# Kernel optimization log

Measured on AMD Instinct MI355X. Metric: run time of the kernel, lower is better.

Reference implementation:

```python
import jax, jax.numpy as jnp
import numpy as np

DH = 5.0       # spatial grid spacing
DT = 0.002     # time step
C  = 2200.0    # wave speed


def setup_inputs() -> dict:
    key = jax.random.key(0)
    # (N, C=1, T, H, W) wavefield snapshots
    inputs = jax.random.normal(key, (8, 1, 64, 256, 256), dtype=jnp.float32)
    return {"inputs": inputs}


def reference(inputs):
    # Effective conv weight is (1,1,3,3,3): single-channel 3x3x3 stencils.
    # padding=(0,1,1): valid along depth (time), zero-pad 1 along H and W.
    u = inputs[:, 0]  # (N, T, H, W)
    up = jnp.pad(u, ((0, 0), (0, 0), (1, 1), (1, 1)))  # zero-pad H, W
    c0 = up[:, 1:-1, 1:-1, 1:-1]  # center tap, (N, T-2, H, W)
    inv_dh2 = 1.0 / (DH * DH)
    inv_dt2 = 1.0 / (DT * DT)
    # [1,-2,1] along W (conv_x kernel)
    u_dxdx = (up[:, 1:-1, 1:-1, :-2] - 2.0 * c0 + up[:, 1:-1, 1:-1, 2:]) * inv_dh2
    # [1,-2,1] along H (conv_y kernel)
    u_dydy = (up[:, 1:-1, :-2, 1:-1] - 2.0 * c0 + up[:, 1:-1, 2:, 1:-1]) * inv_dh2
    # [1,-2,1] along T (conv_z kernel, valid)
    u_dtdt = (up[:, :-2, 1:-1, 1:-1] - 2.0 * c0 + up[:, 2:, 1:-1, 1:-1]) * inv_dt2
    residuals = u_dxdx + u_dydy - u_dtdt * (1.0 / (C * C))
    # torch.norm -> Frobenius norm over all elements
    return jnp.sqrt(jnp.sum(residuals * residuals))
```

## Files before the change

kernel.cpp:

```cpp
#include <hip/hip_runtime.h>
#include <math.h>

#define B_    8
#define T_    64
#define NY_   256
#define NX_   256
#define PS_   (NY_ * NX_)

#define YB_     8
#define NSTRIP  (NY_ / YB_)
#define TCHUNKS 8
#define NWAVES  (B_ * NSTRIP * TCHUNKS)
#define NTHREADS 256
#define NBLOCKS  (NWAVES / 4)

__device__ __forceinline__ float4 loadf4(const float* p) { return *(const float4*)p; }

template <int LEN>
__device__ __forceinline__ float strip_accum(const float* __restrict__ u,
                                             int b, int ys, int t0, int lane) {
    const float a   = 0.04f;
    const float kdt = 250000.0f / 4840000.0f;
    const float k2  = 2.0f * kdt - 4.0f * a;

    const int y0 = ys * YB_;
    const float m0 = (ys > 0)           ? 1.0f : 0.0f;
    const float m5 = (ys < NSTRIP - 1)  ? 1.0f : 0.0f;
    const float xl = (lane > 0)  ? 1.0f : 0.0f;
    const float xr = (lane < 63) ? 1.0f : 0.0f;

    int yoff[YB_ + 2];
    #pragma unroll
    for (int j = 0; j < YB_ + 2; ++j) {
        int y = y0 - 1 + j;
        y = y < 0 ? 0 : (y > NY_ - 1 ? NY_ - 1 : y);
        yoff[j] = y * NX_;
    }

    const float* pl = u + ((size_t)b * T_ + t0) * PS_ + lane * 4;

    float4 tm[YB_], c[YB_ + 2];
    #pragma unroll
    for (int i = 0; i < YB_; ++i) tm[i] = loadf4(pl + yoff[i + 1]);
    const float* p1 = pl + PS_;
    #pragma unroll
    for (int j = 0; j < YB_ + 2; ++j) c[j] = loadf4(p1 + yoff[j]);
    c[0].x *= m0; c[0].y *= m0; c[0].z *= m0; c[0].w *= m0;
    c[YB_+1].x *= m5; c[YB_+1].y *= m5; c[YB_+1].z *= m5; c[YB_+1].w *= m5;

    float acc = 0.0f;
    const float* pn = pl + 2 * PS_;
    #pragma unroll
    for (int k = 0; k < LEN; ++k) {
        float4 nn[YB_ + 2];
        #pragma unroll
        for (int j = 0; j < YB_ + 2; ++j) nn[j] = loadf4(pn + yoff[j]);
        nn[0].x *= m0; nn[0].y *= m0; nn[0].z *= m0; nn[0].w *= m0;
        nn[YB_+1].x *= m5; nn[YB_+1].y *= m5; nn[YB_+1].z *= m5; nn[YB_+1].w *= m5;

        #pragma unroll
        for (int i = 0; i < YB_; ++i) {
            float4 ctr = c[i + 1], up = c[i], dn = c[i + 2];
            float4 t = tm[i], nf = nn[i + 1];
            float cl = __shfl_up(ctr.w, 1, 64) * xl;
            float cr = __shfl_down(ctr.x, 1, 64) * xr;

            {
                float s2 = cl + ctr.y + up.x + dn.x;
                float r = fmaf(s2, a, fmaf(t.x + nf.x, -kdt, ctr.x * k2));
                acc = fmaf(r, r, acc);
            }
            {
                float s2 = ctr.x + ctr.z + up.y + dn.y;
                float r = fmaf(s2, a, fmaf(t.y + nf.y, -kdt, ctr.y * k2));
                acc = fmaf(r, r, acc);
            }
            {
                float s2 = ctr.y + ctr.w + up.z + dn.z;
                float r = fmaf(s2, a, fmaf(t.z + nf.z, -kdt, ctr.z * k2));
                acc = fmaf(r, r, acc);
            }
            {
                float s2 = ctr.z + cr + up.w + dn.w;
                float r = fmaf(s2, a, fmaf(t.w + nf.w, -kdt, ctr.w * k2));
                acc = fmaf(r, r, acc);
            }
        }

        #pragma unroll
        for (int i = 0; i < YB_; ++i) tm[i] = c[i + 1];
        #pragma unroll
        for (int j = 0; j < YB_ + 2; ++j) c[j] = nn[j];
        pn += PS_;
    }
    return acc;
}

__global__ __launch_bounds__(NTHREADS, 2)
void pinn_residual_partial(const float* __restrict__ u, float* __restrict__ partial) {
    const int lane = threadIdx.x & 63;
    const int w    = threadIdx.x >> 6;

    const int b     = blockIdx.x & 7;
    const int inner = blockIdx.x >> 3;
    const int ys    = (inner & 7) * 4 + w;
    const int tc    = inner >> 3;
    const int t0    = tc * 8;

    float s;
    if (tc < TCHUNKS - 1) s = strip_accum<8>(u, b, ys, t0, lane);
    else                  s = strip_accum<6>(u, b, ys, t0, lane);

    #pragma unroll
    for (int off = 32; off > 0; off >>= 1)
        s += __shfl_down(s, off, 64);

    __shared__ float lds[NTHREADS / 64];
    if (lane == 0) lds[w] = s;
    __syncthreads();
    if (threadIdx.x == 0) {
        float bs = lds[0] + lds[1] + lds[2] + lds[3];
        partial[blockIdx.x] = bs;
    }
}

__global__ __launch_bounds__(NTHREADS)
void pinn_finalize(const float* __restrict__ partial, float* __restrict__ out) {
    float s = 0.0f;
    for (int i = threadIdx.x; i < NBLOCKS; i += NTHREADS)
        s += partial[i];
    #pragma unroll
    for (int off = 32; off > 0; off >>= 1)
        s += __shfl_down(s, off, 64);
    __shared__ float lds[NTHREADS / 64];
    int lane = threadIdx.x & 63;
    int wid  = threadIdx.x >> 6;
    if (lane == 0) lds[wid] = s;
    __syncthreads();
    if (threadIdx.x == 0) {
        float bs = 0.0f;
        #pragma unroll
        for (int q = 0; q < NTHREADS / 64; ++q) bs += lds[q];
        out[0] = sqrtf(bs);
    }
}

extern "C" void kernel_launch(void* const* d_in, const int* in_sizes, int n_in,
                              void* d_out, int out_size, void* d_ws, size_t ws_size,
                              hipStream_t stream) {
    const float* u = (const float*)d_in[0];
    float* partial = (float*)d_ws;
    float* out     = (float*)d_out;

    pinn_residual_partial<<<NBLOCKS, NTHREADS, 0, stream>>>(u, partial);
    pinn_finalize<<<1, NTHREADS, 0, stream>>>(partial, out);
}
```

Before: 31.18 us.

## Split each row strip into two x-halves with float2 loads and halo columns

Each wave now covers half a row (128 columns) with float2 loads instead of a full row with float4, so twice as many waves and blocks run. Each lane-0/lane-63 edge gets its neighbour from an extra scalar halo load per row, and the launch bound is raised to 4 blocks per CU so the lighter register footprint allows more occupancy. This is meant to expose more parallelism and latency hiding for a memory-bound stencil, at the cost of extra scalar halo loads and narrower vector accesses.

Result: slower. 43.19 us (+38.5%).

```diff
diff --git a/kernel.cpp b/kernel.cpp
--- a/kernel.cpp
+++ b/kernel.cpp
@@ -10,15 +10,16 @@
 #define YB_     8
 #define NSTRIP  (NY_ / YB_)
 #define TCHUNKS 8
-#define NWAVES  (B_ * NSTRIP * TCHUNKS)
+#define XH_     2
+#define NWAVES  (B_ * NSTRIP * TCHUNKS * XH_)
 #define NTHREADS 256
 #define NBLOCKS  (NWAVES / 4)
 
-__device__ __forceinline__ float4 loadf4(const float* p) { return *(const float4*)p; }
+__device__ __forceinline__ float2 loadf2(const float* p) { return *(const float2*)p; }
 
 template <int LEN>
 __device__ __forceinline__ float strip_accum(const float* __restrict__ u,
-                                             int b, int ys, int t0, int lane) {
+                                             int b, int ys, int t0, int xh, int lane) {
     const float a   = 0.04f;
     const float kdt = 250000.0f / 4840000.0f;
     const float k2  = 2.0f * kdt - 4.0f * a;
@@ -26,8 +27,9 @@
     const int y0 = ys * YB_;
     const float m0 = (ys > 0)           ? 1.0f : 0.0f;
     const float m5 = (ys < NSTRIP - 1)  ? 1.0f : 0.0f;
-    const float xl = (lane > 0)  ? 1.0f : 0.0f;
-    const float xr = (lane < 63) ? 1.0f : 0.0f;
+    const float ehl = (xh != 0) ? 1.0f : 0.0f;
+    const float ehr = 1.0f - ehl;
+    const int   ex  = xh ? 127 : 128;
 
     int yoff[YB_ + 2];
     #pragma unroll
@@ -37,33 +39,44 @@
         yoff[j] = y * NX_;
     }
 
-    const float* pl = u + ((size_t)b * T_ + t0) * PS_ + lane * 4;
+    const float* base = u + ((size_t)b * T_ + t0) * PS_;
+    const float* pl   = base + xh * 128 + lane * 2;
 
-    float4 tm[YB_], c[YB_ + 2];
+    float2 tm[YB_], c[YB_ + 2];
+    float  cE[YB_];
     #pragma unroll
-    for (int i = 0; i < YB_; ++i) tm[i] = loadf4(pl + yoff[i + 1]);
+    for (int i = 0; i < YB_; ++i) tm[i] = loadf2(pl + yoff[i + 1]);
     const float* p1 = pl + PS_;
     #pragma unroll
-    for (int j = 0; j < YB_ + 2; ++j) c[j] = loadf4(p1 + yoff[j]);
-    c[0].x *= m0; c[0].y *= m0; c[0].z *= m0; c[0].w *= m0;
-    c[YB_+1].x *= m5; c[YB_+1].y *= m5; c[YB_+1].z *= m5; c[YB_+1].w *= m5;
+    for (int j = 0; j < YB_ + 2; ++j) c[j] = loadf2(p1 + yoff[j]);
+    const float* e1 = base + PS_;
+    #pragma unroll
+    for (int i = 0; i < YB_; ++i) cE[i] = e1[yoff[i + 1] + ex];
+    c[0].x *= m0; c[0].y *= m0;
+    c[YB_+1].x *= m5; c[YB_+1].y *= m5;
 
     float acc = 0.0f;
     const float* pn = pl + 2 * PS_;
+    const float* pe = base + 2 * PS_;
     #pragma unroll
     for (int k = 0; k < LEN; ++k) {
-        float4 nn[YB_ + 2];
+        float2 nn[YB_ + 2];
+        float  nE[YB_];
         #pragma unroll
-        for (int j = 0; j < YB_ + 2; ++j) nn[j] = loadf4(pn + yoff[j]);
-        nn[0].x *= m0; nn[0].y *= m0; nn[0].z *= m0; nn[0].w *= m0;
-        nn[YB_+1].x *= m5; nn[YB_+1].y *= m5; nn[YB_+1].z *= m5; nn[YB_+1].w *= m5;
+        for (int j = 0; j < YB_ + 2; ++j) nn[j] = loadf2(pn + yoff[j]);
+        #pragma unroll
+        for (int i = 0; i < YB_; ++i) nE[i] = pe[yoff[i + 1] + ex];
+        nn[0].x *= m0; nn[0].y *= m0;
+        nn[YB_+1].x *= m5; nn[YB_+1].y *= m5;
 
         #pragma unroll
         for (int i = 0; i < YB_; ++i) {
-            float4 ctr = c[i + 1], up = c[i], dn = c[i + 2];
-            float4 t = tm[i], nf = nn[i + 1];
-            float cl = __shfl_up(ctr.w, 1, 64) * xl;
-            float cr = __shfl_down(ctr.x, 1, 64) * xr;
+            float2 ctr = c[i + 1], up = c[i], dn = c[i + 2];
+            float2 t = tm[i], nf = nn[i + 1];
+            float clv = __shfl_up(ctr.y, 1, 64);
+            float crv = __shfl_down(ctr.x, 1, 64);
+            float cl = (lane == 0)  ? ehl * cE[i] : clv;
+            float cr = (lane == 63) ? ehr * cE[i] : crv;
 
             {
                 float s2 = cl + ctr.y + up.x + dn.x;
@@ -71,18 +84,8 @@
                 acc = fmaf(r, r, acc);
             }
             {
-                float s2 = ctr.x + ctr.z + up.y + dn.y;
+                float s2 = ctr.x + cr + up.y + dn.y;
                 float r = fmaf(s2, a, fmaf(t.y + nf.y, -kdt, ctr.y * k2));
-                acc = fmaf(r, r, acc);
-            }
-            {
-                float s2 = ctr.y + ctr.w + up.z + dn.z;
-                float r = fmaf(s2, a, fmaf(t.z + nf.z, -kdt, ctr.z * k2));
-                acc = fmaf(r, r, acc);
-            }
-            {
-                float s2 = ctr.z + cr + up.w + dn.w;
-                float r = fmaf(s2, a, fmaf(t.w + nf.w, -kdt, ctr.w * k2));
                 acc = fmaf(r, r, acc);
             }
         }
@@ -91,25 +94,30 @@
         for (int i = 0; i < YB_; ++i) tm[i] = c[i + 1];
         #pragma unroll
         for (int j = 0; j < YB_ + 2; ++j) c[j] = nn[j];
+        #pragma unroll
+        for (int i = 0; i < YB_; ++i) cE[i] = nE[i];
         pn += PS_;
+        pe += PS_;
     }
     return acc;
 }
 
-__global__ __launch_bounds__(NTHREADS, 2)
+__global__ __launch_bounds__(NTHREADS, 4)
 void pinn_residual_partial(const float* __restrict__ u, float* __restrict__ partial) {
     const int lane = threadIdx.x & 63;
     const int w    = threadIdx.x >> 6;
 
     const int b     = blockIdx.x & 7;
     const int inner = blockIdx.x >> 3;
-    const int ys    = (inner & 7) * 4 + w;
-    const int tc    = inner >> 3;
+    const int ysg   = inner & 7;
+    const int xh    = (inner >> 3) & 1;
+    const int tc    = inner >> 4;
+    const int ys    = ysg * 4 + w;
     const int t0    = tc * 8;
 
     float s;
-    if (tc < TCHUNKS - 1) s = strip_accum<8>(u, b, ys, t0, lane);
-    else                  s = strip_accum<6>(u, b, ys, t0, lane);
+    if (tc < TCHUNKS - 1) s = strip_accum<8>(u, b, ys, t0, xh, lane);
+    else                  s = strip_accum<6>(u, b, ys, t0, xh, lane);
 
     #pragma unroll
     for (int off = 32; off > 0; off >>= 1)
```
